# Optimization experiments

Hardware: AMD Instinct MI355X
Metric: run time of the kernel (lower is better)

Reference implementation:

```python
import jax, jax.numpy as jnp
import numpy as np

NEG_SLOPE = 0.2  # PyG GATConv default negative_slope


def gat_layer(x, src, dst, N, W, att_src, att_dst, bias, heads, out_ch, concat):
    # x: [N, Fin]; W: [Fin, heads*out_ch]; att_*: [heads, out_ch]; bias matches output dim
    h = (x @ W).reshape(N, heads, out_ch)              # [N, H, C]
    a_src = (h * att_src).sum(-1)                      # [N, H]
    a_dst = (h * att_dst).sum(-1)                      # [N, H]
    e = jax.nn.leaky_relu(a_src[src] + a_dst[dst], NEG_SLOPE)  # [E, H]
    # segment softmax over incoming edges of each destination node
    e_max = jax.ops.segment_max(e, dst, num_segments=N)        # [N, H]
    e_exp = jnp.exp(e - e_max[dst])                             # [E, H]
    denom = jax.ops.segment_sum(e_exp, dst, num_segments=N)    # [N, H]
    alpha = e_exp / (denom[dst] + 1e-16)                        # [E, H]
    msg = alpha[:, :, None] * h[src]                            # [E, H, C]
    out = jax.ops.segment_sum(msg, dst, num_segments=N)        # [N, H, C]
    out = out.reshape(N, heads * out_ch) if concat else out.mean(axis=1)
    return out + bias


def setup_inputs() -> dict:
    key = jax.random.key(0)
    ks = jax.random.split(key, 10)
    N, E = 40000, 160000
    Fin, H1, C1 = 602, 8, 256
    H2, C2 = 1, 42
    g = lambda k, shape, fan: (jax.random.normal(k, shape, dtype=jnp.float32) * (1.0 / np.sqrt(fan)))
    return {
        "x": jax.random.normal(ks[0], (N, Fin), dtype=jnp.float32),
        "edge_index": jax.random.randint(ks[1], (2, E), 0, N, dtype=jnp.int64),
        "W1": g(ks[2], (Fin, H1 * C1), Fin),
        "att_src1": g(ks[3], (H1, C1), C1),
        "att_dst1": g(ks[4], (H1, C1), C1),
        "b1": jnp.zeros((H1 * C1,), dtype=jnp.float32),
        "W2": g(ks[5], (H1 * C1, H2 * C2), H1 * C1),
        "att_src2": g(ks[6], (H2, C2), C2),
        "att_dst2": g(ks[7], (H2, C2), C2),
        "b2": jnp.zeros((C2,), dtype=jnp.float32),
    }


def reference(x, edge_index, W1, att_src1, att_dst1, b1, W2, att_src2, att_dst2, b2):
    N = x.shape[0]
    # PyG GATConv default add_self_loops=True
    loops = jnp.arange(N, dtype=edge_index.dtype)
    src = jnp.concatenate([edge_index[0], loops])
    dst = jnp.concatenate([edge_index[1], loops])
    h = gat_layer(x, src, dst, N, W1, att_src1, att_dst1, b1, heads=8, out_ch=256, concat=True)
    h = jax.nn.relu(h)  # dropout is identity in eval mode
    h = gat_layer(h, src, dst, N, W2, att_src2, att_dst2, b2, heads=1, out_ch=42, concat=False)
    return jax.nn.log_softmax(h, axis=1)
```

## Files before the change

kernel.cpp:

```cpp
#include <hip/hip_runtime.h>
#include <hip/hip_bf16.h>

#define NN   40000
#define NE   160000
#define ETOT 200000
#define FIN  602
#define NH1  8
#define C1   256
#define F1   2048
#define C2   42
#define NEG  0.2f
#define NB   157
#define KP   608
#define MP   40064

typedef unsigned short u16;
typedef unsigned int   u32;
typedef __bf16 bf16x8 __attribute__((ext_vector_type(8)));
typedef float  f32x4  __attribute__((ext_vector_type(4)));

__device__ __forceinline__ float bfu(u16 v){ return __uint_as_float(((u32)v) << 16); }
__device__ __forceinline__ float bflo(u32 u){ return __uint_as_float(u << 16); }
__device__ __forceinline__ float bfhi(u32 u){ return __uint_as_float(u & 0xffff0000u); }
__device__ __forceinline__ u16 f2bf(float f){
  u32 u = __float_as_uint(f);
  u32 r = (u + 0x7fffu + ((u >> 16) & 1u)) >> 16;
  return (u16)r;
}

__device__ __forceinline__ void gl_lds16(const u16* g, u16* l) {
  __builtin_amdgcn_global_load_lds(
      (const __attribute__((address_space(1))) u32*)(g),
      (__attribute__((address_space(3))) u32*)(l), 16, 0, 0);
}

__global__ void probe_k(const u32* __restrict__ xw, const int* __restrict__ ei,
                        int* __restrict__ flags) {
  if (threadIdx.x == 0) {
    int zc = 0;
    for (int k = 0; k < 64; ++k) zc += (ei[2*k + 1] == 0) ? 1 : 0;
    flags[0] = (zc == 64) ? 1 : 0;
    int inr = 0;
    for (int k = 0; k < 64; ++k) {
      u32 low = xw[k] & 0xffffu;
      int e = (int)((low >> 7) & 0xff);
      inr += (e >= 100 && e <= 140) ? 1 : 0;
    }
    flags[1] = (inr >= 32) ? 0 : 1;
  }
}

__global__ void cvt_f32_k(const void* __restrict__ src, float* __restrict__ dst, int n,
                          const int* __restrict__ flags) {
  int i = blockIdx.x * 256 + threadIdx.x;
  if (i >= n) return;
  dst[i] = flags[1] ? ((const float*)src)[i] : bfu(((const u16*)src)[i]);
}

__global__ void xb_k(const void* __restrict__ x, u16* __restrict__ xb,
                     const int* __restrict__ flags) {
  int k = blockIdx.x * 256 + threadIdx.x;
  int row = blockIdx.y;
  if (k >= KP) return;
  u16 v = 0;
  if (row < NN && k < FIN)
    v = flags[1] ? f2bf(((const float*)x)[(size_t)row * FIN + k])
                 : ((const u16*)x)[(size_t)row * FIN + k];
  xb[(size_t)row * KP + k] = v;
}

__global__ void w1t_k(const void* __restrict__ W1, u16* __restrict__ w1t,
                      const int* __restrict__ flags) {
  int n = blockIdx.x * 256 + threadIdx.x;
  int k = blockIdx.y;
  if (n >= F1) return;
  u16 v = 0;
  if (k < FIN) v = flags[1] ? f2bf(((const float*)W1)[(size_t)k * F1 + n])
                            : ((const u16*)W1)[(size_t)k * F1 + n];
  w1t[(size_t)n * KP + k] = v;
}

__global__ void w2t_k(const void* __restrict__ W2, u16* __restrict__ w2t,
                      const int* __restrict__ flags) {
  int i = blockIdx.x * 256 + threadIdx.x;
  if (i >= 64 * F1) return;
  int c = i >> 11, k = i & (F1 - 1);
  u16 v = 0;
  if (c < C2) v = flags[1] ? f2bf(((const float*)W2)[(size_t)k * C2 + c])
                           : ((const u16*)W2)[(size_t)k * C2 + c];
  w2t[i] = v;
}

__device__ __forceinline__ void edge_sd(const int* __restrict__ ei, int e, int imode,
                                        int& s, int& d) {
  if (e < NE) {
    if (imode) { s = ei[2*e]; d = ei[2*(NE + e)]; }
    else       { s = ei[e];   d = ei[NE + e];     }
  } else { s = d = e - NE; }
}

__global__ void deg_k(const int* __restrict__ ei, int* __restrict__ deg,
                      const int* __restrict__ flags) {
  int e = blockIdx.x * 256 + threadIdx.x;
  if (e >= ETOT) return;
  int s, d; edge_sd(ei, e, flags[0], s, d);
  atomicAdd(&deg[d], 1);
}

__global__ __launch_bounds__(256) void scan1_k(const int* __restrict__ deg,
                                               int* __restrict__ tmp, int* __restrict__ bsum) {
  __shared__ int s[256];
  int b = blockIdx.x, t = threadIdx.x, i = b * 256 + t;
  int v = (i < NN) ? deg[i] : 0;
  s[t] = v; __syncthreads();
  for (int o = 1; o < 256; o <<= 1) {
    int u = (t >= o) ? s[t - o] : 0;
    __syncthreads(); s[t] += u; __syncthreads();
  }
  if (i < NN) tmp[i] = s[t];
  if (t == 255) bsum[b] = s[255];
}

__global__ __launch_bounds__(256) void scan2_k(int* __restrict__ bsum) {
  __shared__ int s[256];
  int t = threadIdx.x;
  int v = (t < NB) ? bsum[t] : 0;
  s[t] = v; __syncthreads();
  for (int o = 1; o < 256; o <<= 1) {
    int u = (t >= o) ? s[t - o] : 0;
    __syncthreads(); s[t] += u; __syncthreads();
  }
  if (t < NB) bsum[t] = s[t];
}

__global__ void scan3_k(const int* __restrict__ deg, const int* __restrict__ tmp,
                        const int* __restrict__ bsum, int* __restrict__ start, int* __restrict__ cur) {
  int i = blockIdx.x * 256 + threadIdx.x;
  if (i >= NN) return;
  int b = i >> 8;
  int off = b ? bsum[b - 1] : 0;
  int excl = tmp[i] - deg[i] + off;
  start[i] = excl; cur[i] = excl;
}

__global__ void fill_k(const int* __restrict__ ei, int* __restrict__ cur,
                       int* __restrict__ csr_src, int* __restrict__ csr_dst,
                       const int* __restrict__ flags) {
  int e = blockIdx.x * 256 + threadIdx.x;
  if (e >= ETOT) return;
  int s, d; edge_sd(ei, e, flags[0], s, d);
  int pos = atomicAdd(&cur[d], 1);
  csr_src[pos] = s; csr_dst[pos] = d;
}

__global__ __launch_bounds__(256) void gemm1a_k(const u16* __restrict__ xb,
                                                const u16* __restrict__ w1t,
                                                u16* __restrict__ h1) {
  __shared__ u16 As[128 * 32];
  __shared__ u16 Bs[128 * 32];
  const int t = threadIdx.x;
  const int lane = t & 63, wid = t >> 6;
  const int wr = wid >> 1, wc = wid & 1;
  const int m0 = blockIdx.y * 128, n0 = blockIdx.x * 128;
  const int l16 = lane & 15, lk = (lane >> 4) * 8;
  f32x4 acc[4][4];
  #pragma unroll
  for (int i = 0; i < 4; ++i)
    #pragma unroll
    for (int j = 0; j < 4; ++j) acc[i][j] = (f32x4){0.f, 0.f, 0.f, 0.f};

  const size_t sa0 = (size_t)(m0 + (t >> 2)) * KP + (t & 3) * 8;
  const size_t sa1 = (size_t)(m0 + 64 + (t >> 2)) * KP + (t & 3) * 8;
  const size_t sb0 = (size_t)(n0 + (t >> 2)) * KP + (t & 3) * 8;
  const size_t sb1 = (size_t)(n0 + 64 + (t >> 2)) * KP + (t & 3) * 8;
  u16* la0 = As + (wid << 9);
  u16* la1 = As + 2048 + (wid << 9);
  u16* lb0 = Bs + (wid << 9);
  u16* lb1 = Bs + 2048 + (wid << 9);

  for (int k0 = 0; k0 < KP; k0 += 32) {
    gl_lds16(xb + sa0 + k0, la0);
    gl_lds16(xb + sa1 + k0, la1);
    gl_lds16(w1t + sb0 + k0, lb0);
    gl_lds16(w1t + sb1 + k0, lb1);
    __syncthreads();
    bf16x8 bfr[4];
    #pragma unroll
    for (int ni = 0; ni < 4; ++ni)
      bfr[ni] = *(const bf16x8*)&Bs[(wc * 64 + ni * 16 + l16) * 32 + lk];
    #pragma unroll
    for (int mi = 0; mi < 4; ++mi) {
      bf16x8 af = *(const bf16x8*)&As[(wr * 64 + mi * 16 + l16) * 32 + lk];
      #pragma unroll
      for (int ni = 0; ni < 4; ++ni)
        acc[mi][ni] = __builtin_amdgcn_mfma_f32_16x16x32_bf16(af, bfr[ni], acc[mi][ni], 0, 0, 0);
    }
    __syncthreads();
  }
  const int lr4 = (lane >> 4) * 4;
  #pragma unroll
  for (int mi = 0; mi < 4; ++mi) {
    #pragma unroll
    for (int r = 0; r < 4; ++r) {
      int row = m0 + wr * 64 + mi * 16 + lr4 + r;
      if (row < NN) {
        #pragma unroll
        for (int ni = 0; ni < 4; ++ni) {
          int col = n0 + wc * 64 + ni * 16 + l16;
          h1[(size_t)row * F1 + col] = f2bf(acc[mi][ni][r]);
        }
      }
    }
  }
}

__global__ __launch_bounds__(256) void gemm1m_k(const void* __restrict__ xv,
                                                const u16* __restrict__ w1t,
                                                u16* __restrict__ h1,
                                                const int* __restrict__ flags) {
  __shared__ u16 As[128][40];
  __shared__ u16 Bs[128][40];
  const int fm = flags[1];
  const int t = threadIdx.x;
  const int lane = t & 63, wid = t >> 6;
  const int wr = wid >> 1, wc = wid & 1;
  const int m0 = blockIdx.y * 128, n0 = blockIdx.x * 128;
  const int l16 = lane & 15, lk = (lane >> 4) * 8;
  f32x4 acc[4][4];
  #pragma unroll
  for (int i = 0; i < 4; ++i)
    #pragma unroll
    for (int j = 0; j < 4; ++j) acc[i][j] = (f32x4){0.f, 0.f, 0.f, 0.f};
  const int arow = t >> 2;
  const int akb  = (t & 3) * 8;
  for (int k0 = 0; k0 < KP; k0 += 32) {
    #pragma unroll
    for (int i = 0; i < 2; ++i) {
      int row = arow + i * 64;
      int rg = m0 + row;
      u32 d0 = 0, d1 = 0, d2 = 0, d3 = 0;
      if (rg < NN) {
        if (k0 + 32 <= FIN) {
          if (fm) {
            const float* xp = (const float*)xv + (size_t)rg * FIN + k0 + akb;
            float2 p0 = *(const float2*)(xp);
            float2 p1 = *(const float2*)(xp + 2);
            float2 p2 = *(const float2*)(xp + 4);
            float2 p3 = *(const float2*)(xp + 6);
            d0 = (u32)f2bf(p0.x) | ((u32)f2bf(p0.y) << 16);
            d1 = (u32)f2bf(p1.x) | ((u32)f2bf(p1.y) << 16);
            d2 = (u32)f2bf(p2.x) | ((u32)f2bf(p2.y) << 16);
            d3 = (u32)f2bf(p3.x) | ((u32)f2bf(p3.y) << 16);
          } else {
            const u16* xp = (const u16*)xv + (size_t)rg * FIN + k0 + akb;
            d0 = *(const u32*)(xp);
            d1 = *(const u32*)(xp + 2);
            d2 = *(const u32*)(xp + 4);
            d3 = *(const u32*)(xp + 6);
          }
        } else {
          u16 e[8];
          #pragma unroll
          for (int q = 0; q < 8; ++q) {
            int k = k0 + akb + q;
            e[q] = 0;
            if (k < FIN)
              e[q] = fm ? f2bf(((const float*)xv)[(size_t)rg * FIN + k])
                        : ((const u16*)xv)[(size_t)rg * FIN + k];
          }
          d0 = (u32)e[0] | ((u32)e[1] << 16);
          d1 = (u32)e[2] | ((u32)e[3] << 16);
          d2 = (u32)e[4] | ((u32)e[5] << 16);
          d3 = (u32)e[6] | ((u32)e[7] << 16);
        }
      }
      *(uint4*)&As[row][akb] = make_uint4(d0, d1, d2, d3);
      const u16* wp = w1t + (size_t)(n0 + row) * KP + k0 + akb;
      *(uint4*)&Bs[row][akb] = *(const uint4*)wp;
    }
    __syncthreads();
    bf16x8 bfr[4];
    #pragma unroll
    for (int ni = 0; ni < 4; ++ni)
      bfr[ni] = *(const bf16x8*)&Bs[wc * 64 + ni * 16 + l16][lk];
    #pragma unroll
    for (int mi = 0; mi < 4; ++mi) {
      bf16x8 af = *(const bf16x8*)&As[wr * 64 + mi * 16 + l16][lk];
      #pragma unroll
      for (int ni = 0; ni < 4; ++ni)
        acc[mi][ni] = __builtin_amdgcn_mfma_f32_16x16x32_bf16(af, bfr[ni], acc[mi][ni], 0, 0, 0);
    }
    __syncthreads();
  }
  const int lr4 = (lane >> 4) * 4;
  #pragma unroll
  for (int mi = 0; mi < 4; ++mi) {
    #pragma unroll
    for (int r = 0; r < 4; ++r) {
      int row = m0 + wr * 64 + mi * 16 + lr4 + r;
      if (row < NN) {
        #pragma unroll
        for (int ni = 0; ni < 4; ++ni) {
          int col = n0 + wc * 64 + ni * 16 + l16;
          h1[(size_t)row * F1 + col] = f2bf(acc[mi][ni][r]);
        }
      }
    }
  }
}

__global__ __launch_bounds__(256) void att1_k(const u16* __restrict__ h1,
                                              const float* __restrict__ as1c, const float* __restrict__ ad1c,
                                              float* __restrict__ a_s, float* __restrict__ a_d) {
  int n = blockIdx.x, t = threadIdx.x;
  int h = t >> 5, l = t & 31;
  int base = h * C1 + l * 8;
  const u16* hp = h1 + (size_t)n * F1 + base;
  uint4 v = *(const uint4*)hp;
  u32 w[4] = {v.x, v.y, v.z, v.w};
  float ss = 0.f, sd = 0.f;
  #pragma unroll
  for (int p = 0; p < 4; ++p) {
    float e0 = bflo(w[p]), e1 = bfhi(w[p]);
    ss += e0 * as1c[base + 2*p] + e1 * as1c[base + 2*p + 1];
    sd += e0 * ad1c[base + 2*p] + e1 * ad1c[base + 2*p + 1];
  }
  #pragma unroll
  for (int o = 16; o > 0; o >>= 1) {
    ss += __shfl_down(ss, o, 32);
    sd += __shfl_down(sd, o, 32);
  }
  if (l == 0) { a_s[n * NH1 + h] = ss; a_d[n * NH1 + h] = sd; }
}

__global__ void ex1_k(const int* __restrict__ csr_src, const int* __restrict__ csr_dst,
                      const float* __restrict__ a_s, const float* __restrict__ a_d,
                      float* __restrict__ ex1) {
  int gid = blockIdx.x * 256 + threadIdx.x;
  if (gid >= ETOT * NH1) return;
  int j = gid >> 3, h = gid & 7;
  float v = a_s[csr_src[j] * NH1 + h] + a_d[csr_dst[j] * NH1 + h];
  v = v > 0.f ? v : NEG * v;
  ex1[gid] = expf(v);
}

__global__ __launch_bounds__(256) void gfuse_k(const int* __restrict__ start, const int* __restrict__ deg,
                                               const int* __restrict__ csr_src, const float* __restrict__ ex1,
                                               const u16* __restrict__ h1, const float* __restrict__ b1c,
                                               const u16* __restrict__ w2t, float* __restrict__ h2) {
  __shared__ u16 rowsL[16 * F1];
  int t = threadIdx.x;
  int nb = blockIdx.x * 16;
  for (int i = 0; i < 16; ++i) {
    int n = nb + i;
    int s0 = start[n], cnt = deg[n];
    float acc[NH1], den[NH1];
    #pragma unroll
    for (int h = 0; h < NH1; ++h) { acc[h] = 0.f; den[h] = 0.f; }
    for (int j = s0; j < s0 + cnt; ++j) {
      int s = csr_src[j];
      const u16* hp = h1 + (size_t)s * F1 + t;
      const float* ep = ex1 + (size_t)j * NH1;
      #pragma unroll
      for (int h = 0; h < NH1; ++h) {
        float e = ep[h];
        den[h] += e;
        acc[h] += e * bfu(hp[h * C1]);
      }
    }
    int sw = (i & 7) << 3;
    #pragma unroll
    for (int h = 0; h < NH1; ++h) {
      float r = acc[h] / (den[h] + 1e-16f) + b1c[h * C1 + t];
      int c = h * C1 + t;
      rowsL[i * F1 + (c ^ sw)] = f2bf(fmaxf(r, 0.f));
    }
  }
  __syncthreads();
  int lane = t & 63, wid = t >> 6;
  int l16 = lane & 15, lk = (lane >> 4) * 8;
  const u16* wt = w2t + (size_t)(wid * 16 + l16) * F1;
  int sw = (l16 & 7) << 3;
  f32x4 acc2 = (f32x4){0.f, 0.f, 0.f, 0.f};
  for (int k0 = 0; k0 < F1; k0 += 32) {
    int kk = k0 + lk;
    bf16x8 af = *(const bf16x8*)&rowsL[l16 * F1 + (kk ^ sw)];
    bf16x8 bf = *(const bf16x8*)(wt + kk);
    acc2 = __builtin_amdgcn_mfma_f32_16x16x32_bf16(af, bf, acc2, 0, 0, 0);
  }
  int col = wid * 16 + l16;
  if (col < C2) {
    int mb = (lane >> 4) * 4;
    #pragma unroll
    for (int r = 0; r < 4; ++r)
      h2[(size_t)(nb + mb + r) * C2 + col] = acc2[r];
  }
}

__global__ __launch_bounds__(64) void att2_k(const float* __restrict__ h2,
                                             const float* __restrict__ as2, const float* __restrict__ ad2,
                                             float* __restrict__ a_s, float* __restrict__ a_d) {
  int n = blockIdx.x, t = threadIdx.x;
  float ss = 0.f, sd = 0.f;
  if (t < C2) {
    float v = h2[(size_t)n * C2 + t];
    ss = v * as2[t];
    sd = v * ad2[t];
  }
  #pragma unroll
  for (int o = 32; o > 0; o >>= 1) {
    ss += __shfl_down(ss, o, 64);
    sd += __shfl_down(sd, o, 64);
  }
  if (t == 0) { a_s[n] = ss; a_d[n] = sd; }
}

__global__ __launch_bounds__(64) void gath2_k(const int* __restrict__ start, const int* __restrict__ deg,
                                              const int* __restrict__ csr_src,
                                              const float* __restrict__ a_s, const float* __restrict__ a_d,
                                              const float* __restrict__ h2, const float* __restrict__ b2,
                                              void* __restrict__ outv, const int* __restrict__ flags) {
  int n = blockIdx.x, t = threadIdx.x;
  int s0 = start[n], cnt = deg[n];
  float ad = a_d[n];
  float acc = 0.f, den = 0.f;
  for (int j = s0; j < s0 + cnt; ++j) {
    int s = csr_src[j];
    float v = a_s[s] + ad;
    v = v > 0.f ? v : NEG * v;
    float e = expf(v);
    den += e;
    if (t < C2) acc += e * h2[(size_t)s * C2 + t];
  }
  float raw = (t < C2) ? acc / (den + 1e-16f) + b2[t] : -1e30f;
  float m = raw;
  #pragma unroll
  for (int o = 32; o > 0; o >>= 1) m = fmaxf(m, __shfl_down(m, o, 64));
  m = __shfl(m, 0, 64);
  float e2 = (t < C2) ? expf(raw - m) : 0.f;
  float ssum = e2;
  #pragma unroll
  for (int o = 32; o > 0; o >>= 1) ssum += __shfl_down(ssum, o, 64);
  ssum = __shfl(ssum, 0, 64);
  if (t < C2) {
    float v = raw - m - logf(ssum);
    if (flags[1]) ((float*)outv)[(size_t)n * C2 + t] = v;
    else          ((u16*) outv)[(size_t)n * C2 + t] = f2bf(v);
  }
}

extern "C" void kernel_launch(void* const* d_in, const int* in_sizes, int n_in,
                              void* d_out, int out_size, void* d_ws, size_t ws_size,
                              hipStream_t stream) {
  const void* x   = d_in[0];
  const int*  ei  = (const int*)d_in[1];
  const void* W1  = d_in[2];
  const void* as1 = d_in[3];
  const void* ad1 = d_in[4];
  const void* b1  = d_in[5];
  const void* W2  = d_in[6];
  const void* as2 = d_in[7];
  const void* ad2 = d_in[8];
  const void* b2  = d_in[9];

  char* ws = (char*)d_ws;
  u16*   h1      = (u16*)  (ws);
  float* ex1     = (float*)(ws + 163840000);
  float* h2      = (float*)(ws + 170240000);
  float* a_s1    = (float*)(ws + 176960000);
  float* a_d1    = (float*)(ws + 178240000);
  float* a_s2    = (float*)(ws + 179520000);
  float* a_d2    = (float*)(ws + 179680000);
  int*   deg     = (int*)  (ws + 179840000);
  int*   start   = (int*)  (ws + 180000000);
  int*   cur     = (int*)  (ws + 180160000);
  int*   tmp     = (int*)  (ws + 180320000);
  int*   csr_src = (int*)  (ws + 180480000);
  int*   csr_dst = (int*)  (ws + 181280000);
  int*   bsum    = (int*)  (ws + 182080000);
  u16*   w1t     = (u16*)  (ws + 182081024);
  u16*   w2t     = (u16*)  (ws + 184571392);
  float* as1c    = (float*)(ws + 184833536);
  float* ad1c    = (float*)(ws + 184841728);
  float* b1c     = (float*)(ws + 184849920);
  float* as2c    = (float*)(ws + 184858112);
  float* ad2c    = (float*)(ws + 184858368);
  float* b2c     = (float*)(ws + 184858624);
  int*   flags   = (int*)  (ws + 184858880);
  const size_t TOTAL_BASE = 184859136;
  u16*   xb      = (u16*)  (ws + TOTAL_BASE);
  const size_t TOTAL_A = TOTAL_BASE + (size_t)MP * KP * 2;
  if (ws_size < TOTAL_BASE) return;
  const bool pathA = (ws_size >= TOTAL_A);

  probe_k<<<1, 64, 0, stream>>>((const u32*)x, ei, flags);

  cvt_f32_k<<<(F1 + 255) / 256, 256, 0, stream>>>(as1, as1c, F1, flags);
  cvt_f32_k<<<(F1 + 255) / 256, 256, 0, stream>>>(ad1, ad1c, F1, flags);
  cvt_f32_k<<<(F1 + 255) / 256, 256, 0, stream>>>(b1, b1c, F1, flags);
  cvt_f32_k<<<1, 256, 0, stream>>>(as2, as2c, C2, flags);
  cvt_f32_k<<<1, 256, 0, stream>>>(ad2, ad2c, C2, flags);
  cvt_f32_k<<<1, 256, 0, stream>>>(b2, b2c, C2, flags);
  w1t_k<<<dim3(8, KP), 256, 0, stream>>>(W1, w1t, flags);
  w2t_k<<<(64 * F1 + 255) / 256, 256, 0, stream>>>(W2, w2t, flags);

  hipMemsetAsync(deg, 0, NN * sizeof(int), stream);
  const int EB = (ETOT + 255) / 256;
  deg_k  <<<EB, 256, 0, stream>>>(ei, deg, flags);
  scan1_k<<<NB, 256, 0, stream>>>(deg, tmp, bsum);
  scan2_k<<<1, 256, 0, stream>>>(bsum);
  scan3_k<<<NB, 256, 0, stream>>>(deg, tmp, bsum, start, cur);
  fill_k <<<EB, 256, 0, stream>>>(ei, cur, csr_src, csr_dst, flags);

  if (pathA) {
    xb_k<<<dim3((KP + 255) / 256, MP), 256, 0, stream>>>(x, xb, flags);
    gemm1a_k<<<dim3(16, MP / 128), 256, 0, stream>>>(xb, w1t, h1);
  } else {
    gemm1m_k<<<dim3(16, MP / 128), 256, 0, stream>>>(x, w1t, h1, flags);
  }
  att1_k<<<NN, 256, 0, stream>>>(h1, as1c, ad1c, a_s1, a_d1);
  ex1_k<<<(ETOT * NH1 + 255) / 256, 256, 0, stream>>>(csr_src, csr_dst, a_s1, a_d1, ex1);
  gfuse_k<<<NN / 16, 256, 0, stream>>>(start, deg, csr_src, ex1, h1, b1c, w2t, h2);

  att2_k<<<NN, 64, 0, stream>>>(h2, as2c, ad2c, a_s2, a_d2);
  gath2_k<<<NN, 64, 0, stream>>>(start, deg, csr_src, a_s2, a_d2, h2, b2c, d_out, flags);
}
```

Before: 623.1 us.

## Fuse attention logits into GEMM epilogue and compute edge weights inside aggregation

The first GEMM now computes the per-head source and destination attention dot products in its epilogue, reducing them with shuffles and atomics into zeroed buffers, so the separate att1 pass that re-read h1 is dropped on the main path. The ex1 kernel is removed and the aggregation kernel computes leaky-relu and exp per edge on the fly. The gather is also reworked so each thread loads 8 contiguous bf16 features with one 16-byte load, processing two edges per iteration and writing packed output to LDS. In exchange it adds float atomics, whose order makes the sums non-deterministic, plus an extra memset and redundant exp work per thread in each head group.

Result: slower. 655.1 us (+5.1%).

```diff
diff --git a/kernel.cpp b/kernel.cpp
--- a/kernel.cpp
+++ b/kernel.cpp
@@ -155,7 +155,11 @@
 
 __global__ __launch_bounds__(256) void gemm1a_k(const u16* __restrict__ xb,
                                                 const u16* __restrict__ w1t,
-                                                u16* __restrict__ h1) {
+                                                u16* __restrict__ h1,
+                                                const float* __restrict__ as1c,
+                                                const float* __restrict__ ad1c,
+                                                float* __restrict__ a_s1,
+                                                float* __restrict__ a_d1) {
   __shared__ u16 As[128 * 32];
   __shared__ u16 Bs[128 * 32];
   const int t = threadIdx.x;
@@ -197,7 +201,50 @@
     }
     __syncthreads();
   }
+
+  const int h0 = n0 >> 8;
+  float psrc[4][4], pdst[4][4];
+  #pragma unroll
+  for (int mi = 0; mi < 4; ++mi)
+    #pragma unroll
+    for (int r = 0; r < 4; ++r) { psrc[mi][r] = 0.f; pdst[mi][r] = 0.f; }
+  #pragma unroll
+  for (int ni = 0; ni < 4; ++ni) {
+    int col = n0 + wc * 64 + ni * 16 + l16;
+    float wsv = as1c[col], wdv = ad1c[col];
+    #pragma unroll
+    for (int mi = 0; mi < 4; ++mi)
+      #pragma unroll
+      for (int r = 0; r < 4; ++r) {
+        float v = acc[mi][ni][r];
+        psrc[mi][r] += v * wsv;
+        pdst[mi][r] += v * wdv;
+      }
+  }
+  #pragma unroll
+  for (int o = 1; o < 16; o <<= 1) {
+    #pragma unroll
+    for (int mi = 0; mi < 4; ++mi)
+      #pragma unroll
+      for (int r = 0; r < 4; ++r) {
+        psrc[mi][r] += __shfl_xor(psrc[mi][r], o, 64);
+        pdst[mi][r] += __shfl_xor(pdst[mi][r], o, 64);
+      }
+  }
   const int lr4 = (lane >> 4) * 4;
+  if (l16 == 0) {
+    #pragma unroll
+    for (int mi = 0; mi < 4; ++mi)
+      #pragma unroll
+      for (int r = 0; r < 4; ++r) {
+        int row = m0 + wr * 64 + mi * 16 + lr4 + r;
+        if (row < NN) {
+          atomicAdd(&a_s1[row * NH1 + h0], psrc[mi][r]);
+          atomicAdd(&a_d1[row * NH1 + h0], pdst[mi][r]);
+        }
+      }
+  }
+
   #pragma unroll
   for (int mi = 0; mi < 4; ++mi) {
     #pragma unroll
@@ -333,48 +380,71 @@
   if (l == 0) { a_s[n * NH1 + h] = ss; a_d[n * NH1 + h] = sd; }
 }
 
-__global__ void ex1_k(const int* __restrict__ csr_src, const int* __restrict__ csr_dst,
-                      const float* __restrict__ a_s, const float* __restrict__ a_d,
-                      float* __restrict__ ex1) {
-  int gid = blockIdx.x * 256 + threadIdx.x;
-  if (gid >= ETOT * NH1) return;
-  int j = gid >> 3, h = gid & 7;
-  float v = a_s[csr_src[j] * NH1 + h] + a_d[csr_dst[j] * NH1 + h];
-  v = v > 0.f ? v : NEG * v;
-  ex1[gid] = expf(v);
-}
-
 __global__ __launch_bounds__(256) void gfuse_k(const int* __restrict__ start, const int* __restrict__ deg,
-                                               const int* __restrict__ csr_src, const float* __restrict__ ex1,
+                                               const int* __restrict__ csr_src,
+                                               const float* __restrict__ a_s1, const float* __restrict__ a_d1,
                                                const u16* __restrict__ h1, const float* __restrict__ b1c,
                                                const u16* __restrict__ w2t, float* __restrict__ h2) {
   __shared__ u16 rowsL[16 * F1];
   int t = threadIdx.x;
   int nb = blockIdx.x * 16;
+  int h = t >> 5;
+  int c0 = t * 8;
+  float4 bA = *(const float4*)(b1c + c0);
+  float4 bB = *(const float4*)(b1c + c0 + 4);
   for (int i = 0; i < 16; ++i) {
     int n = nb + i;
-    int s0 = start[n], cnt = deg[n];
-    float acc[NH1], den[NH1];
-    #pragma unroll
-    for (int h = 0; h < NH1; ++h) { acc[h] = 0.f; den[h] = 0.f; }
-    for (int j = s0; j < s0 + cnt; ++j) {
-      int s = csr_src[j];
-      const u16* hp = h1 + (size_t)s * F1 + t;
-      const float* ep = ex1 + (size_t)j * NH1;
-      #pragma unroll
-      for (int h = 0; h < NH1; ++h) {
-        float e = ep[h];
-        den[h] += e;
-        acc[h] += e * bfu(hp[h * C1]);
-      }
-    }
+    int s0 = start[n], jend = s0 + deg[n];
+    float ad = a_d1[n * NH1 + h];
+    float a0=0.f,a1=0.f,a2=0.f,a3=0.f,a4=0.f,a5=0.f,a6=0.f,a7=0.f,den=0.f;
+    int j = s0;
+    for (; j + 2 <= jend; j += 2) {
+      int sA = csr_src[j], sB = csr_src[j + 1];
+      float vA = a_s1[sA * NH1 + h] + ad;
+      float vB = a_s1[sB * NH1 + h] + ad;
+      vA = vA > 0.f ? vA : NEG * vA;
+      vB = vB > 0.f ? vB : NEG * vB;
+      float eA = expf(vA), eB = expf(vB);
+      uint4 uA = *(const uint4*)(h1 + (size_t)sA * F1 + c0);
+      uint4 uB = *(const uint4*)(h1 + (size_t)sB * F1 + c0);
+      den += eA + eB;
+      a0 += eA * bflo(uA.x) + eB * bflo(uB.x);
+      a1 += eA * bfhi(uA.x) + eB * bfhi(uB.x);
+      a2 += eA * bflo(uA.y) + eB * bflo(uB.y);
+      a3 += eA * bfhi(uA.y) + eB * bfhi(uB.y);
+      a4 += eA * bflo(uA.z) + eB * bflo(uB.z);
+      a5 += eA * bfhi(uA.z) + eB * bfhi(uB.z);
+      a6 += eA * bflo(uA.w) + eB * bflo(uB.w);
+      a7 += eA * bfhi(uA.w) + eB * bfhi(uB.w);
+    }
+    if (j < jend) {
+      int sA = csr_src[j];
+      float vA = a_s1[sA * NH1 + h] + ad;
+      vA = vA > 0.f ? vA : NEG * vA;
+      float eA = expf(vA);
+      uint4 uA = *(const uint4*)(h1 + (size_t)sA * F1 + c0);
+      den += eA;
+      a0 += eA * bflo(uA.x); a1 += eA * bfhi(uA.x);
+      a2 += eA * bflo(uA.y); a3 += eA * bfhi(uA.y);
+      a4 += eA * bflo(uA.z); a5 += eA * bfhi(uA.z);
+      a6 += eA * bflo(uA.w); a7 += eA * bfhi(uA.w);
+    }
+    float inv = 1.f / (den + 1e-16f);
+    u16 o0 = f2bf(fmaxf(a0 * inv + bA.x, 0.f));
+    u16 o1 = f2bf(fmaxf(a1 * inv + bA.y, 0.f));
+    u16 o2 = f2bf(fmaxf(a2 * inv + bA.z, 0.f));
+    u16 o3 = f2bf(fmaxf(a3 * inv + bA.w, 0.f));
+    u16 o4 = f2bf(fmaxf(a4 * inv + bB.x, 0.f));
+    u16 o5 = f2bf(fmaxf(a5 * inv + bB.y, 0.f));
+    u16 o6 = f2bf(fmaxf(a6 * inv + bB.z, 0.f));
+    u16 o7 = f2bf(fmaxf(a7 * inv + bB.w, 0.f));
+    uint4 pk;
+    pk.x = (u32)o0 | ((u32)o1 << 16);
+    pk.y = (u32)o2 | ((u32)o3 << 16);
+    pk.z = (u32)o4 | ((u32)o5 << 16);
+    pk.w = (u32)o6 | ((u32)o7 << 16);
     int sw = (i & 7) << 3;
-    #pragma unroll
-    for (int h = 0; h < NH1; ++h) {
-      float r = acc[h] / (den[h] + 1e-16f) + b1c[h * C1 + t];
-      int c = h * C1 + t;
-      rowsL[i * F1 + (c ^ sw)] = f2bf(fmaxf(r, 0.f));
-    }
+    *(uint4*)&rowsL[i * F1 + (c0 ^ sw)] = pk;
   }
   __syncthreads();
   int lane = t & 63, wid = t >> 6;
@@ -492,6 +562,7 @@
   const size_t TOTAL_A = TOTAL_BASE + (size_t)MP * KP * 2;
   if (ws_size < TOTAL_BASE) return;
   const bool pathA = (ws_size >= TOTAL_A);
+  (void)ex1;
 
   probe_k<<<1, 64, 0, stream>>>((const u32*)x, ei, flags);
 
@@ -505,6 +576,7 @@
   w2t_k<<<(64 * F1 + 255) / 256, 256, 0, stream>>>(W2, w2t, flags);
 
   hipMemsetAsync(deg, 0, NN * sizeof(int), stream);
+  hipMemsetAsync(a_s1, 0, 2 * NN * NH1 * sizeof(float), stream);
   const int EB = (ETOT + 255) / 256;
   deg_k  <<<EB, 256, 0, stream>>>(ei, deg, flags);
   scan1_k<<<NB, 256, 0, stream>>>(deg, tmp, bsum);
@@ -514,13 +586,12 @@
 
   if (pathA) {
     xb_k<<<dim3((KP + 255) / 256, MP), 256, 0, stream>>>(x, xb, flags);
-    gemm1a_k<<<dim3(16, MP / 128), 256, 0, stream>>>(xb, w1t, h1);
+    gemm1a_k<<<dim3(16, MP / 128), 256, 0, stream>>>(xb, w1t, h1, as1c, ad1c, a_s1, a_d1);
   } else {
     gemm1m_k<<<dim3(16, MP / 128), 256, 0, stream>>>(x, w1t, h1, flags);
-  }
-  att1_k<<<NN, 256, 0, stream>>>(h1, as1c, ad1c, a_s1, a_d1);
-  ex1_k<<<(ETOT * NH1 + 255) / 256, 256, 0, stream>>>(csr_src, csr_dst, a_s1, a_d1, ex1);
-  gfuse_k<<<NN / 16, 256, 0, stream>>>(start, deg, csr_src, ex1, h1, b1c, w2t, h2);
+    att1_k<<<NN, 256, 0, stream>>>(h1, as1c, ad1c, a_s1, a_d1);
+  }
+  gfuse_k<<<NN / 16, 256, 0, stream>>>(start, deg, csr_src, a_s1, a_d1, h1, b1c, w2t, h2);
 
   att2_k<<<NN, 64, 0, stream>>>(h2, as2c, ad2c, a_s2, a_d2);
   gath2_k<<<NN, 64, 0, stream>>>(start, deg, csr_src, a_s2, a_d2, h2, b2c, d_out, flags);
```
